# Performance work log

Measured on AMD Instinct MI355X. Metric: run time of the kernel, lower is better.

The kernel has to match this reference:

```python
import jax, jax.numpy as jnp
import numpy as np

D_MODEL = 1024
N_LAYER = 2
VOCAB = 50257
D_STATE = 64
D_CONV = 4
EXPAND = 2
HEADDIM = 64
D_INNER = EXPAND * D_MODEL            # 2048
NHEADS = D_INNER // HEADDIM           # 32
CONV_DIM = D_INNER + 2 * D_STATE      # x, B, C share the conv (ngroups=1)
D_PROJ = 2 * D_INNER + 2 * D_STATE + NHEADS  # z, xBC, dt
D_FF = 4 * D_MODEL
B, T = 1, 1024
EPS = 1e-5


def _layernorm(x, w):
    mu = jnp.mean(x, -1, keepdims=True)
    v = jnp.mean((x - mu) ** 2, -1, keepdims=True)
    return (x - mu) * jax.lax.rsqrt(v + EPS) * w


def _rmsnorm(x, w):
    return x * jax.lax.rsqrt(jnp.mean(x ** 2, -1, keepdims=True) + EPS) * w


def setup_inputs() -> dict:
    key = jax.random.key(0)
    ks = jax.random.split(key, 16)
    std = 0.02
    idx = jax.random.randint(ks[0], (B, T), 0, VOCAB)
    targets = jax.random.randint(ks[1], (B, T), 0, VOCAB)
    E = jax.random.normal(ks[2], (VOCAB, D_MODEL)) * std  # tied embedding / lm_head
    norm_w = jnp.ones((N_LAYER, D_MODEL))
    norm2_w = jnp.ones((N_LAYER, D_MODEL))
    norm_f_w = jnp.ones((D_MODEL,))
    in_proj_w = jax.random.normal(ks[3], (N_LAYER, D_PROJ, D_MODEL)) * std
    conv_w = jax.random.normal(ks[4], (N_LAYER, CONV_DIM, D_CONV)) / np.sqrt(D_CONV)
    conv_b = jnp.zeros((N_LAYER, CONV_DIM))
    dt = jnp.exp(jax.random.uniform(ks[5], (N_LAYER, NHEADS)) * (np.log(0.1) - np.log(1e-3)) + np.log(1e-3))
    dt_bias = dt + jnp.log(-jnp.expm1(-dt))  # inverse softplus
    A_log = jnp.log(jax.random.uniform(ks[6], (N_LAYER, NHEADS), minval=1.0, maxval=16.0))
    Dp = jnp.ones((N_LAYER, NHEADS))
    gnorm_w = jnp.ones((N_LAYER, D_INNER))
    out_proj_w = jax.random.normal(ks[7], (N_LAYER, D_MODEL, D_INNER)) * std / np.sqrt(2 * N_LAYER)
    fc1_w = jax.random.normal(ks[8], (N_LAYER, 2 * D_FF, D_MODEL)) * std
    fc2_w = jax.random.normal(ks[9], (N_LAYER, D_MODEL, D_FF)) * std / np.sqrt(2 * N_LAYER)
    return {"idx": idx, "targets": targets, "E": E, "norm_w": norm_w, "norm2_w": norm2_w,
            "in_proj_w": in_proj_w, "conv_w": conv_w, "conv_b": conv_b, "dt_bias": dt_bias,
            "A_log": A_log, "Dp": Dp, "gnorm_w": gnorm_w, "out_proj_w": out_proj_w,
            "fc1_w": fc1_w, "fc2_w": fc2_w, "norm_f_w": norm_f_w}


def _mamba2(x, Wi, cw, cb, dtb, Al, Dh, gw, Wo):
    b, l, _ = x.shape
    zxbcdt = x @ Wi.T  # [b,l,D_PROJ]
    z = zxbcdt[..., :D_INNER]
    xBC = zxbcdt[..., D_INNER:D_INNER + CONV_DIM]
    dt = zxbcdt[..., D_INNER + CONV_DIM:]  # [b,l,H]
    # depthwise causal conv1d over time
    xp = jnp.pad(xBC, ((0, 0), (D_CONV - 1, 0), (0, 0)))
    xBC = sum(xp[:, k:k + l, :] * cw[:, k] for k in range(D_CONV)) + cb
    xBC = jax.nn.silu(xBC)
    xs = xBC[..., :D_INNER].reshape(b, l, NHEADS, HEADDIM)
    Bm = xBC[..., D_INNER:D_INNER + D_STATE]  # [b,l,N] (ngroups=1)
    Cm = xBC[..., D_INNER + D_STATE:]
    dt = jax.nn.softplus(dt + dtb)            # [b,l,H]
    dA = jnp.exp(dt * (-jnp.exp(Al)))         # [b,l,H]
    tm = lambda a: jnp.moveaxis(a, 1, 0)      # time-major for scan

    def step(h, inp):
        dA_t, dt_t, x_t, B_t, C_t = inp
        h = dA_t[..., None, None] * h + jnp.einsum('bh,bhp,bn->bhpn', dt_t, x_t, B_t)
        return h, jnp.einsum('bhpn,bn->bhp', h, C_t)

    h0 = jnp.zeros((b, NHEADS, HEADDIM, D_STATE), x.dtype)
    _, ys = jax.lax.scan(step, h0, (tm(dA), tm(dt), tm(xs), tm(Bm), tm(Cm)))
    y = jnp.moveaxis(ys, 0, 1) + Dh[None, None, :, None] * xs  # skip term D*x
    y = y.reshape(b, l, D_INNER)
    y = _rmsnorm(y * jax.nn.silu(z), gw)  # gated RMSNorm
    return y @ Wo.T


def _gated_mlp(x, W1, W2):
    y = x @ W1.T
    y, g = jnp.split(y, 2, axis=-1)
    return (y * jax.nn.silu(g)) @ W2.T


def reference(idx, targets, E, norm_w, norm2_w, in_proj_w, conv_w, conv_b, dt_bias,
              A_log, Dp, gnorm_w, out_proj_w, fc1_w, fc2_w, norm_f_w):
    h = E[idx]  # [B,T,D]
    for i in range(N_LAYER):
        x = _layernorm(h, norm_w[i])
        x = _mamba2(x, in_proj_w[i], conv_w[i], conv_b[i], dt_bias[i], A_log[i],
                    Dp[i], gnorm_w[i], out_proj_w[i])
        res = x + h
        x = _layernorm(res, norm2_w[i])
        h = _gated_mlp(x, fc1_w[i], fc2_w[i]) + res
    h = _layernorm(h, norm_f_w)
    logits = h @ E.T  # tied lm_head
    logp = jax.nn.log_softmax(logits, axis=-1)
    nll = -jnp.take_along_axis(logp, targets[..., None], axis=-1)[..., 0]
    loss = jnp.mean(nll)  # no ignore_index=-1 entries present
    return logits, loss
```

## Files before the change

kernel.cpp:

```cpp
#include <hip/hip_runtime.h>
#include <cmath>

#define DMODEL  1024
#define DINNER  2048
#define NHEADS  32
#define CONVDIM 2176
#define DPROJ   4256
#define VOCAB   50257
#define NBLK_V  400
#define VOCABP  (NBLK_V * 128)
#define CLEN    16
#define NCHUNK  64

typedef float f32x4 __attribute__((ext_vector_type(4)));
typedef float f32x2 __attribute__((ext_vector_type(2)));
typedef unsigned short u16;
typedef u16 u16x4 __attribute__((ext_vector_type(4)));
typedef u16 u16x8 __attribute__((ext_vector_type(8)));
typedef __bf16 bf16x8 __attribute__((ext_vector_type(8)));

__device__ __forceinline__ u16 f2bf(float f) {
  unsigned u = __builtin_bit_cast(unsigned, f);
  u += 0x7FFFu + ((u >> 16) & 1u);
  return (u16)(u >> 16);
}
__device__ __forceinline__ float silu_f(float x) { return x / (1.f + expf(-x)); }

__device__ __forceinline__ void gload16(const u16* g, u16* l) {
  __builtin_amdgcn_global_load_lds(
      (const __attribute__((address_space(1))) void*)g,
      (__attribute__((address_space(3))) void*)l,
      16, 0, 0);
}

__global__ __launch_bounds__(256) void gemm_bf16(
    const u16* __restrict__ A, const u16* __restrict__ B,
    float* __restrict__ C, int N, int K, int kslice,
    float* __restrict__ lsepart, int swz, int nblk,
    u16* __restrict__ glu_out)
{
  __shared__ alignas(128) u16 As[3 * 4096];
  __shared__ alignas(128) u16 Bs[3 * 4096];
  const int tid = threadIdx.x;
  int m0, n0;
  if (swz) {
    int bid = blockIdx.x;
    m0 = ((bid >> 3) & 7) << 7;
    n0 = ((bid & 7) + ((bid >> 6) << 3)) << 7;
  } else {
    m0 = blockIdx.x << 7;
    n0 = blockIdx.y << 7;
  }
  const int lane = tid & 63, wid = tid >> 6;
  const int wm = (wid >> 1) << 6, wn = (wid & 1) << 6;
  const int lr = lane & 15, kg = lane >> 4;

  const int srow = wid * 16 + (lane >> 2);
  const int scol = ((lane & 3) ^ ((lane >> 3) & 3)) << 3;
  const u16* gA = A + (size_t)(m0 + srow) * K + scol;
  const u16* gB = B + (size_t)(n0 + srow) * K + scol;

  f32x4 acc[4][4];
#pragma unroll
  for (int i = 0; i < 4; ++i)
#pragma unroll
    for (int j = 0; j < 4; ++j) acc[i][j] = (f32x4){0.f, 0.f, 0.f, 0.f};

  const int kb = blockIdx.z * kslice;
  const int nt = kslice >> 5;

  auto stage = [&](int buf, int t) {
    const int ko = kb + (t << 5);
#pragma unroll
    for (int i = 0; i < 2; ++i) {
      gload16(gA + ko + (size_t)i * 64 * K, &As[buf * 4096 + i * 2048 + wid * 512]);
      gload16(gB + ko + (size_t)i * 64 * K, &Bs[buf * 4096 + i * 2048 + wid * 512]);
    }
  };

  stage(0, 0);
  stage(1, 1);
  int b0 = 0, b1 = 1, b2 = 2;
  const int cxr = ((lr >> 1) & 3);
  for (int t = 0; t < nt; ++t) {
    if (t == nt - 1) asm volatile("s_waitcnt vmcnt(0)" ::: "memory");
    else             asm volatile("s_waitcnt vmcnt(4)" ::: "memory");
    __builtin_amdgcn_s_barrier();
    if (t + 2 < nt) stage(b2, t + 2);
    bf16x8 af[4], bfr[4];
#pragma unroll
    for (int f = 0; f < 4; ++f) {
      const int po = ((kg ^ cxr) << 3);
      af[f]  = *(const bf16x8*)&As[b0 * 4096 + (wm + f * 16 + lr) * 32 + po];
      bfr[f] = *(const bf16x8*)&Bs[b0 * 4096 + (wn + f * 16 + lr) * 32 + po];
    }
#pragma unroll
    for (int i = 0; i < 4; ++i)
#pragma unroll
      for (int j = 0; j < 4; ++j)
        acc[i][j] = __builtin_amdgcn_mfma_f32_16x16x32_bf16(af[i], bfr[j], acc[i][j], 0, 0, 0);
    int tmp = b0; b0 = b1; b1 = b2; b2 = tmp;
  }

  const int mr = (lane >> 4) << 2;
  const int nc = lane & 15;

  if (glu_out) {
#pragma unroll
    for (int i = 0; i < 4; ++i)
#pragma unroll
      for (int j = 0; j < 4; ++j)
#pragma unroll
        for (int e = 0; e < 4; ++e) {
          float v = acc[i][j][e];
          float p = __shfl_xor(v, 1);
          if (!(nc & 1)) {
            int q = (n0 + wn + j * 16 + nc) >> 1;
            int row = m0 + wm + i * 16 + mr + e;
            glu_out[(size_t)row * 4096 + q] = f2bf(v * silu_f(p));
          }
        }
    return;
  }

  float* Cw = C + (gridDim.z > 1 ? (size_t)blockIdx.z * 1024 * N : 0);
#pragma unroll
  for (int i = 0; i < 4; ++i)
#pragma unroll
    for (int j = 0; j < 4; ++j) {
      int n = n0 + wn + j * 16 + nc;
      if (n < N) {
#pragma unroll
        for (int e = 0; e < 4; ++e)
          Cw[(size_t)(m0 + wm + i * 16 + mr + e) * N + n] = acc[i][j][e];
      }
    }

  if (lsepart) {
    __syncthreads();
    float* Ls = (float*)As;
#pragma unroll
    for (int i = 0; i < 4; ++i)
#pragma unroll
      for (int e = 0; e < 4; ++e) {
        float pm = -1e30f;
#pragma unroll
        for (int j = 0; j < 4; ++j) {
          int n = n0 + wn + j * 16 + nc;
          if (n < N) pm = fmaxf(pm, acc[i][j][e]);
        }
#pragma unroll
        for (int o = 1; o < 16; o <<= 1) pm = fmaxf(pm, __shfl_xor(pm, o));
        float ps = 0.f;
#pragma unroll
        for (int j = 0; j < 4; ++j) {
          int n = n0 + wn + j * 16 + nc;
          if (n < N) ps += expf(acc[i][j][e] - pm);
        }
#pragma unroll
        for (int o = 1; o < 16; o <<= 1) ps += __shfl_xor(ps, o);
        if (nc == 0) {
          int row = wm + i * 16 + mr + e;
          Ls[row * 4 + (wid & 1) * 2] = pm;
          Ls[row * 4 + (wid & 1) * 2 + 1] = ps;
        }
      }
    __syncthreads();
    if (tid < 128) {
      float pa = Ls[tid * 4], sa = Ls[tid * 4 + 1];
      float pb = Ls[tid * 4 + 2], sb = Ls[tid * 4 + 3];
      float M = fmaxf(pa, pb);
      float S = sa * expf(pa - M) + sb * expf(pb - M);
      ((f32x2*)lsepart)[(size_t)(m0 + tid) * nblk + (n0 >> 7)] = (f32x2){M, S};
    }
  }
}

__global__ void k_cvt8(const float* __restrict__ src, u16* __restrict__ dst, int n8) {
  int i = blockIdx.x * 256 + threadIdx.x;
  if (i >= n8) return;
  f32x4 a = ((const f32x4*)src)[i * 2];
  f32x4 b = ((const f32x4*)src)[i * 2 + 1];
  u16x8 o = { f2bf(a[0]), f2bf(a[1]), f2bf(a[2]), f2bf(a[3]),
              f2bf(b[0]), f2bf(b[1]), f2bf(b[2]), f2bf(b[3]) };
  ((u16x8*)dst)[i] = o;
}

__global__ void k_cvt8_pad(const float* __restrict__ src, u16* __restrict__ dst,
                           int n8, int srcN8) {
  int i = blockIdx.x * 256 + threadIdx.x;
  if (i >= n8) return;
  u16x8 o;
  if (i < srcN8) {
    f32x4 a = ((const f32x4*)src)[i * 2];
    f32x4 b = ((const f32x4*)src)[i * 2 + 1];
    o = (u16x8){ f2bf(a[0]), f2bf(a[1]), f2bf(a[2]), f2bf(a[3]),
                 f2bf(b[0]), f2bf(b[1]), f2bf(b[2]), f2bf(b[3]) };
  } else {
    o = (u16x8){0, 0, 0, 0, 0, 0, 0, 0};
  }
  ((u16x8*)dst)[i] = o;
}

__global__ void k_cvt_fc1(const float* __restrict__ src, u16* __restrict__ dst, int n8) {
  int i = blockIdx.x * 256 + threadIdx.x;
  if (i >= n8) return;
  f32x4 a = ((const f32x4*)src)[i * 2];
  f32x4 b = ((const f32x4*)src)[i * 2 + 1];
  u16x8 o = { f2bf(a[0]), f2bf(a[1]), f2bf(a[2]), f2bf(a[3]),
              f2bf(b[0]), f2bf(b[1]), f2bf(b[2]), f2bf(b[3]) };
  int R = i >> 7, col8 = i & 127;
  int layer = R >> 13, r = R & 8191;
  int dstr = (r < 4096) ? (r << 1) : (((r - 4096) << 1) | 1);
  ((u16x8*)dst)[((size_t)(layer << 13) + dstr) * 128 + col8] = o;
}

__device__ __forceinline__ void ln_write(f32x4 v, const float* __restrict__ w,
                                         u16* __restrict__ out, int t, int tid) {
  float s = v[0] + v[1] + v[2] + v[3];
  float sq = v[0]*v[0] + v[1]*v[1] + v[2]*v[2] + v[3]*v[3];
#pragma unroll
  for (int o = 32; o; o >>= 1) { s += __shfl_down(s, o); sq += __shfl_down(sq, o); }
  __shared__ float sb[4], qb[4];
  if ((tid & 63) == 0) { sb[tid >> 6] = s; qb[tid >> 6] = sq; }
  __syncthreads();
  s = sb[0] + sb[1] + sb[2] + sb[3];
  sq = qb[0] + qb[1] + qb[2] + qb[3];
  float mu = s * (1.f / 1024.f);
  float rstd = rsqrtf(sq * (1.f / 1024.f) - mu * mu + 1e-5f);
  u16x4 o;
#pragma unroll
  for (int e = 0; e < 4; ++e) o[e] = f2bf((v[e] - mu) * rstd * w[tid * 4 + e]);
  ((u16x4*)out)[t * 256 + tid] = o;
}

__global__ void k_ln_embed(const int* __restrict__ idx, const float* __restrict__ E,
                           const float* __restrict__ w, float* __restrict__ hbuf,
                           u16* __restrict__ out) {
  int t = blockIdx.x, tid = threadIdx.x;
  f32x4 v = ((const f32x4*)(E + (size_t)idx[t] * DMODEL))[tid];
  ((f32x4*)hbuf)[t * 256 + tid] = v;
  ln_write(v, w, out, t, tid);
}

__global__ void k_red_ln(const float* __restrict__ part, int S,
                         float* __restrict__ hbuf, const float* __restrict__ w,
                         u16* __restrict__ out) {
  int t = blockIdx.x, tid = threadIdx.x;
  f32x4 v = ((const f32x4*)hbuf)[t * 256 + tid];
  for (int k = 0; k < S; ++k)
    v += ((const f32x4*)part)[(size_t)k * 262144 + t * 256 + tid];
  ((f32x4*)hbuf)[t * 256 + tid] = v;
  ln_write(v, w, out, t, tid);
}

__global__ void k_convdt(const float* __restrict__ zx, const float* __restrict__ cw,
                         const float* __restrict__ cb, const float* __restrict__ dtb,
                         const float* __restrict__ alog, float* __restrict__ xbc,
                         float* __restrict__ dtsp, float* __restrict__ dag) {
  int t = blockIdx.y, x = blockIdx.x, tid = threadIdx.x;
  if (x < 8 || tid < 128) {
    int c = x * 256 + tid;
    float acc = cb[c];
#pragma unroll
    for (int k = 0; k < 4; ++k) {
      int tt = t + k - 3;
      if (tt >= 0) acc += zx[(size_t)tt * DPROJ + 2048 + c] * cw[c * 4 + k];
    }
    xbc[(size_t)t * CONVDIM + c] = silu_f(acc);
  } else if (tid < 160) {
    int hh = tid - 128;
    float raw = zx[(size_t)t * DPROJ + 4224 + hh] + dtb[hh];
    float sp = raw > 20.f ? raw : log1pf(expf(raw));
    dtsp[t * 32 + hh] = sp;
    dag[t * 32 + hh] = expf(-expf(alog[hh]) * sp);
  }
}

__global__ __launch_bounds__(256) void k_scan_local(
    const float* __restrict__ xbc, const float* __restrict__ dtsp,
    const float* __restrict__ dag, float* __restrict__ yb, float* __restrict__ Sloc,
    float* __restrict__ pref, float* __restrict__ dacum)
{
  int c = blockIdx.x, hh = blockIdx.y;
  int tid = threadIdx.x;
  int p = tid >> 2, ng = tid & 3, n0 = ng << 4;
  float st[16];
#pragma unroll
  for (int j = 0; j < 16; ++j) st[j] = 0.f;
  float P = 1.f;
  for (int s_ = 0; s_ < CLEN; ++s_) {
    int t = c * CLEN + s_;
    float dA = dag[t * 32 + hh];
    P *= dA;
    if (tid == 0) pref[t * 32 + hh] = P;
    float coef = dtsp[t * 32 + hh] * xbc[(size_t)t * CONVDIM + hh * 64 + p];
    const f32x4* B4 = (const f32x4*)&xbc[(size_t)t * CONVDIM + 2048 + n0];
    const f32x4* C4 = (const f32x4*)&xbc[(size_t)t * CONVDIM + 2112 + n0];
    float y = 0.f;
#pragma unroll
    for (int q = 0; q < 4; ++q) {
      f32x4 b = B4[q], cc = C4[q];
#pragma unroll
      for (int e = 0; e < 4; ++e) {
        int j = q * 4 + e;
        st[j] = dA * st[j] + coef * b[e];
        y += st[j] * cc[e];
      }
    }
    y += __shfl_xor(y, 1);
    y += __shfl_xor(y, 2);
    if (ng == 0) yb[(size_t)t * DINNER + hh * 64 + p] = y;
  }
  if (tid == 0) dacum[c * 32 + hh] = P;
  float* Sp = Sloc + ((size_t)(c * 32 + hh) * 64 + p) * 64 + n0;
#pragma unroll
  for (int q = 0; q < 4; ++q)
    *(f32x4*)(Sp + q * 4) = (f32x4){ st[q*4], st[q*4+1], st[q*4+2], st[q*4+3] };
}

__global__ void k_chain(const float* __restrict__ Sloc, const float* __restrict__ dacum,
                        float* __restrict__ Sin) {
  int e = blockIdx.x * 256 + threadIdx.x;
  int hh = e >> 12;
  float S = 0.f;
  for (int c = 0; c < NCHUNK; c += 8) {
    float sl[8], dd[8];
#pragma unroll
    for (int j = 0; j < 8; ++j) sl[j] = Sloc[(size_t)(c + j) * 131072 + e];
#pragma unroll
    for (int j = 0; j < 8; ++j) dd[j] = dacum[(c + j) * 32 + hh];
#pragma unroll
    for (int j = 0; j < 8; ++j) {
      Sin[(size_t)(c + j) * 131072 + e] = S;
      S = dd[j] * S + sl[j];
    }
  }
}

__global__ __launch_bounds__(256) void k_scan_fix(
    const float* __restrict__ xbc, const float* __restrict__ pref,
    const float* __restrict__ Sin, const float* __restrict__ Dp,
    float* __restrict__ yb)
{
  __shared__ float Sl[64 * 68];
  int c = blockIdx.x, hh = blockIdx.y;
  int tid = threadIdx.x;
  for (int i = 0; i < 16; ++i) {
    int e = i * 256 + tid;
    Sl[(e >> 6) * 68 + (e & 63)] = Sin[(size_t)(c * 32 + hh) * 4096 + e];
  }
  __syncthreads();
  int p = tid >> 2, ng = tid & 3, n0 = ng << 4;
  float Dh = Dp[hh];
  for (int s_ = 0; s_ < CLEN; ++s_) {
    int t = c * CLEN + s_;
    const f32x4* C4 = (const f32x4*)&xbc[(size_t)t * CONVDIM + 2112 + n0];
    float yc = 0.f;
#pragma unroll
    for (int q = 0; q < 4; ++q) {
      f32x4 cc = C4[q];
#pragma unroll
      for (int e = 0; e < 4; ++e) yc += Sl[p * 68 + n0 + q * 4 + e] * cc[e];
    }
    yc += __shfl_xor(yc, 1);
    yc += __shfl_xor(yc, 2);
    if (ng == 0) {
      size_t oy = (size_t)t * DINNER + hh * 64 + p;
      yb[oy] = yb[oy] + pref[t * 32 + hh] * yc + Dh * xbc[(size_t)t * CONVDIM + hh * 64 + p];
    }
  }
}

__global__ void k_gated_rms(const float* __restrict__ yb, const float* __restrict__ zx,
                            const float* __restrict__ gw, u16* __restrict__ out) {
  int t = blockIdx.x, tid = threadIdx.x;
  float v[8], ss = 0.f;
#pragma unroll
  for (int i = 0; i < 8; ++i) {
    int j = tid + i * 256;
    float z = zx[(size_t)t * DPROJ + j];
    float vv = yb[(size_t)t * DINNER + j] * silu_f(z);
    v[i] = vv; ss += vv * vv;
  }
#pragma unroll
  for (int o = 32; o; o >>= 1) ss += __shfl_down(ss, o);
  __shared__ float sb[4];
  if ((tid & 63) == 0) sb[tid >> 6] = ss;
  __syncthreads();
  ss = sb[0] + sb[1] + sb[2] + sb[3];
  float rstd = rsqrtf(ss * (1.f / 2048.f) + 1e-5f);
#pragma unroll
  for (int i = 0; i < 8; ++i) {
    int j = tid + i * 256;
    out[(size_t)t * DINNER + j] = f2bf(v[i] * rstd * gw[j]);
  }
}

__global__ void k_loss_final(const float* __restrict__ lsepart,
                             const float* __restrict__ logits,
                             const int* __restrict__ tgt, float* __restrict__ part) {
  int t = blockIdx.x, tid = threadIdx.x;
  float m = -1e30f, s = 0.f;
  for (int nb = tid; nb < NBLK_V; nb += 256) {
    f32x2 v = ((const f32x2*)lsepart)[(size_t)t * NBLK_V + nb];
    float M = fmaxf(m, v[0]);
    s = s * expf(m - M) + v[1] * expf(v[0] - M);
    m = M;
  }
#pragma unroll
  for (int o = 32; o; o >>= 1) {
    float m2 = __shfl_down(m, o), s2 = __shfl_down(s, o);
    float M = fmaxf(m, m2);
    s = s * expf(m - M) + s2 * expf(m2 - M);
    m = M;
  }
  __shared__ float ms[4], ssh[4];
  if ((tid & 63) == 0) { ms[tid >> 6] = m; ssh[tid >> 6] = s; }
  __syncthreads();
  if (tid == 0) {
    float M = ms[0], S = ssh[0];
    for (int w = 1; w < 4; ++w) {
      float M2 = fmaxf(M, ms[w]);
      S = S * expf(M - M2) + ssh[w] * expf(ms[w] - M2);
      M = M2;
    }
    part[t] = (M + logf(S)) - logits[(size_t)t * VOCAB + tgt[t]];
  }
}

__global__ void k_loss_mean(const float* __restrict__ part, float* __restrict__ out) {
  int tid = threadIdx.x;
  float s = 0.f;
  for (int j = tid; j < 1024; j += 256) s += part[j];
#pragma unroll
  for (int o = 32; o; o >>= 1) s += __shfl_down(s, o);
  __shared__ float sb[4];
  if ((tid & 63) == 0) sb[tid >> 6] = s;
  __syncthreads();
  if (tid == 0) out[0] = (sb[0] + sb[1] + sb[2] + sb[3]) * (1.f / 1024.f);
}

extern "C" void kernel_launch(void* const* d_in, const int* in_sizes, int n_in,
                              void* d_out, int out_size, void* d_ws, size_t ws_size,
                              hipStream_t stream)
{
  const int*   idx       = (const int*)d_in[0];
  const int*   tgt       = (const int*)d_in[1];
  const float* E         = (const float*)d_in[2];
  const float* norm_w    = (const float*)d_in[3];
  const float* norm2_w   = (const float*)d_in[4];
  const float* in_proj_w = (const float*)d_in[5];
  const float* conv_w    = (const float*)d_in[6];
  const float* conv_b    = (const float*)d_in[7];
  const float* dt_bias   = (const float*)d_in[8];
  const float* A_log     = (const float*)d_in[9];
  const float* Dp        = (const float*)d_in[10];
  const float* gnorm_w   = (const float*)d_in[11];
  const float* out_proj_w= (const float*)d_in[12];
  const float* fc1_w     = (const float*)d_in[13];
  const float* fc2_w     = (const float*)d_in[14];
  const float* norm_f_w  = (const float*)d_in[15];
  float* logits = (float*)d_out;
  (void)in_sizes; (void)n_in; (void)out_size; (void)ws_size;

  char* W = (char*)d_ws;
  size_t off = 0;
  auto A8 = [&](size_t bytes) { void* p = W + off; off = (off + bytes + 255) & ~(size_t)255; return p; };
  float* hbuf   = (float*)A8((size_t)1024 * 1024 * 4);
  u16*   xnormb = (u16*)  A8((size_t)1024 * 1024 * 2);
  u16*   gatedb = (u16*)  A8((size_t)1024 * 2048 * 2);
  u16*   glub   = (u16*)  A8((size_t)1024 * 4096 * 2);
  float* dtsp   = (float*)A8((size_t)1024 * 32 * 4);
  float* dag    = (float*)A8((size_t)1024 * 32 * 4);
  float* pref   = (float*)A8((size_t)1024 * 32 * 4);
  float* dacum  = (float*)A8((size_t)2048 * 4);
  float* lpart  = (float*)A8((size_t)1024 * 4);
  float* lsebuf = (float*)A8((size_t)1024 * NBLK_V * 2 * 4);
  u16*   wip    = (u16*)  A8((size_t)2 * 4352 * 1024 * 2);
  u16*   wop    = (u16*)  A8((size_t)2 * 1024 * 2048 * 2);
  u16*   wfc1   = (u16*)  A8((size_t)2 * 8192 * 1024 * 2);
  u16*   wfc2   = (u16*)  A8((size_t)2 * 1024 * 4096 * 2);
  char*  span   = (char*)A8((size_t)117964800);
  float* big0   = (float*)(span);
  float* xbc    = (float*)(span + 33554432);
  float* yb     = (float*)(span + 33554432 + 8912896);
  float* Sloc   = (float*)(span + 33554432 + 8912896 + 8388608);
  float* Sin    = (float*)((char*)Sloc + 33554432);
  float* part   = Sloc;
  u16*   Ebf    = (u16*)span;

  dim3 b256(256);

  k_cvt8_pad<<<dim3((4352*1024/8 + 255)/256), b256, 0, stream>>>(
      in_proj_w, wip, 4352*1024/8, 4256*1024/8);
  k_cvt8_pad<<<dim3((4352*1024/8 + 255)/256), b256, 0, stream>>>(
      in_proj_w + (size_t)4256*1024, wip + (size_t)4352*1024, 4352*1024/8, 4256*1024/8);
  k_cvt8<<<dim3(2*1024*2048/8/256), b256, 0, stream>>>(out_proj_w, wop, 2*1024*2048/8);
  k_cvt_fc1<<<dim3(2*8192*1024/8/256), b256, 0, stream>>>(fc1_w, wfc1, 2*8192*1024/8);
  k_cvt8<<<dim3(2*1024*4096/8/256), b256, 0, stream>>>(fc2_w, wfc2, 2*1024*4096/8);

  k_ln_embed<<<1024, b256, 0, stream>>>(idx, E, norm_w, hbuf, xnormb);

  const float* nw_next[2] = { norm_w + 1024, norm_f_w };
  for (int L = 0; L < 2; ++L) {
    gemm_bf16<<<dim3(8, 34, 1), b256, 0, stream>>>(
        xnormb, wip + (size_t)L * 4352 * 1024, big0, DPROJ, 1024, 1024,
        nullptr, 0, 34, nullptr);
    k_convdt<<<dim3(9, 1024), b256, 0, stream>>>(
        big0, conv_w + L * CONVDIM * 4, conv_b + L * CONVDIM,
        dt_bias + L * 32, A_log + L * 32, xbc, dtsp, dag);
    k_scan_local<<<dim3(64, 32), b256, 0, stream>>>(xbc, dtsp, dag, yb, Sloc, pref, dacum);
    k_chain<<<512, b256, 0, stream>>>(Sloc, dacum, Sin);
    k_scan_fix<<<dim3(64, 32), b256, 0, stream>>>(xbc, pref, Sin, Dp + L * 32, yb);
    k_gated_rms<<<1024, b256, 0, stream>>>(yb, big0, gnorm_w + L * 2048, gatedb);
    gemm_bf16<<<dim3(8, 8, 4), b256, 0, stream>>>(
        gatedb, wop + (size_t)L * 1024 * 2048, part, 1024, 2048, 512,
        nullptr, 0, 8, nullptr);
    k_red_ln<<<1024, b256, 0, stream>>>(part, 4, hbuf, norm2_w + L * 1024, xnormb);
    gemm_bf16<<<dim3(8, 64, 1), b256, 0, stream>>>(
        xnormb, wfc1 + (size_t)L * 8192 * 1024, nullptr, 8192, 1024, 1024,
        nullptr, 0, 64, glub);
    gemm_bf16<<<dim3(8, 8, 8), b256, 0, stream>>>(
        glub, wfc2 + (size_t)L * 1024 * 4096, part, 1024, 4096, 512,
        nullptr, 0, 8, nullptr);
    k_red_ln<<<1024, b256, 0, stream>>>(part, 8, hbuf, nw_next[L], xnormb);
  }

  k_cvt8_pad<<<dim3((VOCABP*1024/8 + 255)/256), b256, 0, stream>>>(
      E, Ebf, VOCABP*1024/8, VOCAB*1024/8);
  gemm_bf16<<<dim3(8 * NBLK_V, 1, 1), b256, 0, stream>>>(
      xnormb, Ebf, logits, VOCAB, 1024, 1024, lsebuf, 1, NBLK_V, nullptr);
  k_loss_final<<<1024, b256, 0, stream>>>(lsebuf, logits, tgt, lpart);
  k_loss_mean<<<1, b256, 0, stream>>>(lpart, logits + (size_t)1024 * VOCAB);
}
```

Measured before the change: 823.9 us.

## Add 256x128-tile GEMM for fc1 and lm_head, double scan chunk length

Introduces a 512-thread GEMM kernel whose tile is 256 rows by 128 columns. It is used for the fc1 GLU GEMM and the tied lm_head GEMM with the fused log-sum-exp partials, so each B-tile load is reused across twice as many rows and B traffic from global memory drops. The original kernel is stripped down to plain stores. The SSM chunk length also changes from 16 to 32, halving the chunk count, which shifts work from the inter-chunk chain into the local scans. The larger tile needs more LDS and registers per block, which may lower occupancy.

```diff
diff --git a/kernel.cpp b/kernel.cpp
--- a/kernel.cpp
+++ b/kernel.cpp
@@ -9,8 +9,8 @@
 #define VOCAB   50257
 #define NBLK_V  400
 #define VOCABP  (NBLK_V * 128)
-#define CLEN    16
-#define NCHUNK  64
+#define CLEN    32
+#define NCHUNK  32
 
 typedef float f32x4 __attribute__((ext_vector_type(4)));
 typedef float f32x2 __attribute__((ext_vector_type(2)));
@@ -35,22 +35,13 @@
 
 __global__ __launch_bounds__(256) void gemm_bf16(
     const u16* __restrict__ A, const u16* __restrict__ B,
-    float* __restrict__ C, int N, int K, int kslice,
-    float* __restrict__ lsepart, int swz, int nblk,
-    u16* __restrict__ glu_out)
+    float* __restrict__ C, int N, int K, int kslice)
 {
   __shared__ alignas(128) u16 As[3 * 4096];
   __shared__ alignas(128) u16 Bs[3 * 4096];
   const int tid = threadIdx.x;
-  int m0, n0;
-  if (swz) {
-    int bid = blockIdx.x;
-    m0 = ((bid >> 3) & 7) << 7;
-    n0 = ((bid & 7) + ((bid >> 6) << 3)) << 7;
-  } else {
-    m0 = blockIdx.x << 7;
-    n0 = blockIdx.y << 7;
-  }
+  const int m0 = blockIdx.x << 7;
+  const int n0 = blockIdx.y << 7;
   const int lane = tid & 63, wid = tid >> 6;
   const int wm = (wid >> 1) << 6, wn = (wid & 1) << 6;
   const int lr = lane & 15, kg = lane >> 4;
@@ -88,10 +79,92 @@
     __builtin_amdgcn_s_barrier();
     if (t + 2 < nt) stage(b2, t + 2);
     bf16x8 af[4], bfr[4];
+    const int po = ((kg ^ cxr) << 3);
 #pragma unroll
     for (int f = 0; f < 4; ++f) {
-      const int po = ((kg ^ cxr) << 3);
       af[f]  = *(const bf16x8*)&As[b0 * 4096 + (wm + f * 16 + lr) * 32 + po];
+      bfr[f] = *(const bf16x8*)&Bs[b0 * 4096 + (wn + f * 16 + lr) * 32 + po];
+    }
+#pragma unroll
+    for (int i = 0; i < 4; ++i)
+#pragma unroll
+      for (int j = 0; j < 4; ++j)
+        acc[i][j] = __builtin_amdgcn_mfma_f32_16x16x32_bf16(af[i], bfr[j], acc[i][j], 0, 0, 0);
+    int tmp = b0; b0 = b1; b1 = b2; b2 = tmp;
+  }
+
+  const int mr = (lane >> 4) << 2;
+  const int nc = lane & 15;
+  float* Cw = C + (gridDim.z > 1 ? (size_t)blockIdx.z * 1024 * N : 0);
+#pragma unroll
+  for (int i = 0; i < 4; ++i)
+#pragma unroll
+    for (int j = 0; j < 4; ++j) {
+      int n = n0 + wn + j * 16 + nc;
+      if (n < N) {
+#pragma unroll
+        for (int e = 0; e < 4; ++e)
+          Cw[(size_t)(m0 + wm + i * 16 + mr + e) * N + n] = acc[i][j][e];
+      }
+    }
+}
+
+__global__ __launch_bounds__(512) void gemm256(
+    const u16* __restrict__ A, const u16* __restrict__ B,
+    float* __restrict__ C, int N, int K,
+    float* __restrict__ lsepart, int swz, int nblk,
+    u16* __restrict__ glu_out)
+{
+  __shared__ alignas(128) u16 As[3 * 8192];
+  __shared__ alignas(128) u16 Bs[3 * 4096];
+  const int tid = threadIdx.x;
+  int m0, n0;
+  if (swz) {
+    int bid = blockIdx.x;
+    m0 = ((bid >> 3) & 3) << 8;
+    n0 = ((bid & 7) + ((bid >> 5) << 3)) << 7;
+  } else {
+    m0 = blockIdx.x << 8;
+    n0 = blockIdx.y << 7;
+  }
+  const int lane = tid & 63, wid = tid >> 6;
+  const int wm = (wid >> 1) << 6, wn = (wid & 1) << 6;
+  const int lr = lane & 15, kg = lane >> 4;
+
+  const int srow = wid * 16 + (lane >> 2);
+  const int scol = ((lane & 3) ^ ((lane >> 3) & 3)) << 3;
+  const u16* gA = A + (size_t)(m0 + srow) * K + scol;
+  const u16* gB = B + (size_t)(n0 + srow) * K + scol;
+
+  f32x4 acc[4][4];
+#pragma unroll
+  for (int i = 0; i < 4; ++i)
+#pragma unroll
+    for (int j = 0; j < 4; ++j) acc[i][j] = (f32x4){0.f, 0.f, 0.f, 0.f};
+
+  const int nt = K >> 5;
+
+  auto stage = [&](int buf, int t) {
+    const int ko = t << 5;
+    gload16(gA + ko,                     &As[buf * 8192 + wid * 512]);
+    gload16(gA + ko + (size_t)128 * K,   &As[buf * 8192 + 4096 + wid * 512]);
+    gload16(gB + ko,                     &Bs[buf * 4096 + wid * 512]);
+  };
+
+  stage(0, 0);
+  stage(1, 1);
+  int b0 = 0, b1 = 1, b2 = 2;
+  const int cxr = ((lr >> 1) & 3);
+  for (int t = 0; t < nt; ++t) {
+    if (t == nt - 1) asm volatile("s_waitcnt vmcnt(0)" ::: "memory");
+    else             asm volatile("s_waitcnt vmcnt(3)" ::: "memory");
+    __builtin_amdgcn_s_barrier();
+    if (t + 2 < nt) stage(b2, t + 2);
+    bf16x8 af[4], bfr[4];
+    const int po = ((kg ^ cxr) << 3);
+#pragma unroll
+    for (int f = 0; f < 4; ++f) {
+      af[f]  = *(const bf16x8*)&As[b0 * 8192 + (wm + f * 16 + lr) * 32 + po];
       bfr[f] = *(const bf16x8*)&Bs[b0 * 4096 + (wn + f * 16 + lr) * 32 + po];
     }
 #pragma unroll
@@ -123,7 +196,6 @@
     return;
   }
 
-  float* Cw = C + (gridDim.z > 1 ? (size_t)blockIdx.z * 1024 * N : 0);
 #pragma unroll
   for (int i = 0; i < 4; ++i)
 #pragma unroll
@@ -132,7 +204,7 @@
       if (n < N) {
 #pragma unroll
         for (int e = 0; e < 4; ++e)
-          Cw[(size_t)(m0 + wm + i * 16 + mr + e) * N + n] = acc[i][j][e];
+          C[(size_t)(m0 + wm + i * 16 + mr + e) * N + n] = acc[i][j][e];
       }
     }
 
@@ -166,7 +238,7 @@
         }
       }
     __syncthreads();
-    if (tid < 128) {
+    if (tid < 256) {
       float pa = Ls[tid * 4], sa = Ls[tid * 4 + 1];
       float pb = Ls[tid * 4 + 2], sb = Ls[tid * 4 + 3];
       float M = fmaxf(pa, pb);
@@ -490,7 +562,7 @@
   float* part   = Sloc;
   u16*   Ebf    = (u16*)span;
 
-  dim3 b256(256);
+  dim3 b256(256), b512(512);
 
   k_cvt8_pad<<<dim3((4352*1024/8 + 255)/256), b256, 0, stream>>>(
       in_proj_w, wip, 4352*1024/8, 4256*1024/8);
@@ -505,32 +577,29 @@
   const float* nw_next[2] = { norm_w + 1024, norm_f_w };
   for (int L = 0; L < 2; ++L) {
     gemm_bf16<<<dim3(8, 34, 1), b256, 0, stream>>>(
-        xnormb, wip + (size_t)L * 4352 * 1024, big0, DPROJ, 1024, 1024,
-        nullptr, 0, 34, nullptr);
+        xnormb, wip + (size_t)L * 4352 * 1024, big0, DPROJ, 1024, 1024);
     k_convdt<<<dim3(9, 1024), b256, 0, stream>>>(
         big0, conv_w + L * CONVDIM * 4, conv_b + L * CONVDIM,
         dt_bias + L * 32, A_log + L * 32, xbc, dtsp, dag);
-    k_scan_local<<<dim3(64, 32), b256, 0, stream>>>(xbc, dtsp, dag, yb, Sloc, pref, dacum);
+    k_scan_local<<<dim3(NCHUNK, 32), b256, 0, stream>>>(xbc, dtsp, dag, yb, Sloc, pref, dacum);
     k_chain<<<512, b256, 0, stream>>>(Sloc, dacum, Sin);
-    k_scan_fix<<<dim3(64, 32), b256, 0, stream>>>(xbc, pref, Sin, Dp + L * 32, yb);
+    k_scan_fix<<<dim3(NCHUNK, 32), b256, 0, stream>>>(xbc, pref, Sin, Dp + L * 32, yb);
     k_gated_rms<<<1024, b256, 0, stream>>>(yb, big0, gnorm_w + L * 2048, gatedb);
     gemm_bf16<<<dim3(8, 8, 4), b256, 0, stream>>>(
-        gatedb, wop + (size_t)L * 1024 * 2048, part, 1024, 2048, 512,
-        nullptr, 0, 8, nullptr);
+        gatedb, wop + (size_t)L * 1024 * 2048, part, 1024, 2048, 512);
     k_red_ln<<<1024, b256, 0, stream>>>(part, 4, hbuf, norm2_w + L * 1024, xnormb);
-    gemm_bf16<<<dim3(8, 64, 1), b256, 0, stream>>>(
-        xnormb, wfc1 + (size_t)L * 8192 * 1024, nullptr, 8192, 1024, 1024,
+    gemm256<<<dim3(4, 64, 1), b512, 0, stream>>>(
+        xnormb, wfc1 + (size_t)L * 8192 * 1024, nullptr, 8192, 1024,
         nullptr, 0, 64, glub);
     gemm_bf16<<<dim3(8, 8, 8), b256, 0, stream>>>(
-        glub, wfc2 + (size_t)L * 1024 * 4096, part, 1024, 4096, 512,
-        nullptr, 0, 8, nullptr);
+        glub, wfc2 + (size_t)L * 1024 * 4096, part, 1024, 4096, 512);
     k_red_ln<<<1024, b256, 0, stream>>>(part, 8, hbuf, nw_next[L], xnormb);
   }
 
   k_cvt8_pad<<<dim3((VOCABP*1024/8 + 255)/256), b256, 0, stream>>>(
       E, Ebf, VOCABP*1024/8, VOCAB*1024/8);
-  gemm_bf16<<<dim3(8 * NBLK_V, 1, 1), b256, 0, stream>>>(
-      xnormb, Ebf, logits, VOCAB, 1024, 1024, lsebuf, 1, NBLK_V, nullptr);
+  gemm256<<<dim3(4 * NBLK_V, 1, 1), b512, 0, stream>>>(
+      xnormb, Ebf, logits, VOCAB, 1024, lsebuf, 1, NBLK_V, nullptr);
   k_loss_final<<<1024, b256, 0, stream>>>(lsebuf, logits, tgt, lpart);
   k_loss_mean<<<1, b256, 0, stream>>>(lpart, logits + (size_t)1024 * VOCAB);
 }
```

New measurement: 786.0 us. -4.6%, faster.
